# Kernel tuning notes

Hardware: AMD Instinct MI355X
Metric: run time of the kernel (lower is better)

The kernel has to match this reference:

```python
import jax, jax.numpy as jnp
import numpy as np

D_MODEL, N_HEADS, HEAD_DIM, MAX_POS = 1536, 16, 96, 4096
B, T = 2, 2048
BASE = 10000.0


def build_rope3d_Rs(head_dim, max_pos, base=BASE):
    """Rodrigues rotations R(t) = exp(t*M_k): (max_pos, n_trip, 3, 3)."""
    n_trip = head_dim // 3
    inv_freq = base ** (-np.arange(n_trip, dtype=np.float64) * 2.0 / head_dim)
    Ms = np.zeros((n_trip, 3, 3), dtype=np.float64)
    for k in range(n_trip):  # tiny fixed loop (n_trip=32)
        m, axis = inv_freq[k], k % 3
        if axis == 0:
            Ms[k, 0, 1], Ms[k, 1, 0] = m, -m
        elif axis == 1:
            Ms[k, 1, 2], Ms[k, 2, 1] = m, -m
        else:
            Ms[k, 0, 2], Ms[k, 2, 0] = m, -m
    m_s = np.abs(Ms).max(axis=(1, 2))                      # (n_trip,)
    pos = np.arange(max_pos, dtype=np.float64)
    ang = pos[:, None] * m_s[None, :]                      # (P, n_trip)
    Mu = Ms / np.maximum(m_s, 1e-30)[:, None, None]
    Mu2 = np.einsum('kij,kjl->kil', Mu, Mu)
    Rs = (np.eye(3)[None, None]
          + np.sin(ang)[..., None, None] * Mu[None]
          + (1.0 - np.cos(ang))[..., None, None] * Mu2[None])
    return jnp.asarray(Rs, dtype=jnp.float32)


def setup_inputs() -> dict:
    key = jax.random.key(0)
    kx, kq, ko = jax.random.split(key, 3)
    s_in = 1.0 / np.sqrt(D_MODEL)
    s_out = 1.0 / np.sqrt(N_HEADS * HEAD_DIM)
    return {
        'x': jax.random.normal(kx, (B, T, D_MODEL), dtype=jnp.float32),
        'w_qkv': jax.random.normal(kq, (3 * N_HEADS * HEAD_DIM, D_MODEL), dtype=jnp.float32) * s_in,
        'w_o': jax.random.normal(ko, (D_MODEL, N_HEADS * HEAD_DIM), dtype=jnp.float32) * s_out,
        'Rs': build_rope3d_Rs(HEAD_DIM, MAX_POS),
    }


def apply_rope3d(x, Rs):
    # x: (B,H,T,d); Rs: (P, n_trip, 3, 3), d = 3*n_trip
    b, h, t, d = x.shape
    xg = x.reshape(b, h, t, d // 3, 3)
    out = jnp.einsum('tkij,bhtkj->bhtki', Rs[:t], xg)
    return out.reshape(b, h, t, d)


def reference(x, w_qkv, w_o, Rs):
    b, t, _ = x.shape
    qkv = (x @ w_qkv.T).reshape(b, t, 3, N_HEADS, HEAD_DIM)
    qkv = jnp.transpose(qkv, (2, 0, 3, 1, 4))              # (3,B,H,T,hd)
    q, k, v = qkv[0], qkv[1], qkv[2]
    q = apply_rope3d(q, Rs)
    k = apply_rope3d(k, Rs)
    scale = 1.0 / jnp.sqrt(jnp.asarray(HEAD_DIM, dtype=x.dtype))
    scores = jnp.einsum('bhqd,bhkd->bhqk', q, k) * scale   # (B,H,T,T)
    causal = jnp.tril(jnp.ones((t, t), dtype=bool))
    scores = jnp.where(causal, scores, jnp.finfo(x.dtype).min)
    att = jax.nn.softmax(scores, axis=-1)
    out = jnp.einsum('bhqk,bhkd->bhqd', att, v)            # (B,H,T,hd)
    out = jnp.transpose(out, (0, 2, 1, 3)).reshape(b, t, N_HEADS * HEAD_DIM)
    return out @ w_o.T
```

## Files before the change

### kernel.cpp

```cpp
#include <hip/hip_runtime.h>
#include <stdint.h>


typedef unsigned short u16;
typedef unsigned int u32;
typedef __attribute__((ext_vector_type(8))) __bf16 bf16x8;
typedef __attribute__((ext_vector_type(4))) float f32x4;

#define DEV static __device__ __forceinline__

DEV u16 f2bf(float f) {
  u32 u = __float_as_uint(f);
  return (u16)((u + 0x7fffu + ((u >> 16) & 1u)) >> 16);
}
DEV float bf2f(u16 h) { return __uint_as_float(((u32)h) << 16); }
DEV u32 cvtpk(float lo, float hi) {
  u32 r;
  asm("v_cvt_pk_bf16_f32 %0, %1, %2" : "=v"(r) : "v"(lo), "v"(hi));
  return r;
}
DEV float exp2f_fast(float x) {
  float r;
  asm("v_exp_f32 %0, %1" : "=v"(r) : "v"(x));
  return r;
}

DEV void gload16(u16* lds_dst, const u16* gsrc) {
  __builtin_amdgcn_global_load_lds(
      (const __attribute__((address_space(1))) void*)gsrc,
      (__attribute__((address_space(3))) void*)lds_dst, 16, 0, 0);
}

__global__ __launch_bounds__(256) void cvt_bf16(const float* __restrict__ in,
                                                u16* __restrict__ out, int n4) {
  int i = blockIdx.x * 256 + threadIdx.x;
  if (i < n4) {
    float4 v = reinterpret_cast<const float4*>(in)[i];
    ushort4 o;
    o.x = f2bf(v.x); o.y = f2bf(v.y); o.z = f2bf(v.z); o.w = f2bf(v.w);
    reinterpret_cast<ushort4*>(out)[i] = o;
  }
}

template <int OUT_BF16>
__global__ __launch_bounds__(512, 4) void gemm_bal(const u16* __restrict__ A,
                                                   const u16* __restrict__ B,
                                                   void* __restrict__ Cv,
                                                   int M, int N, int K) {
  (void)M;
  __shared__ __align__(16) u16 sA[2][128 * 64];
  __shared__ __align__(16) u16 sB[2][192 * 64];
  const int tid = threadIdx.x;
  const int lane = tid & 63, w = tid >> 6;
  const int wm = w >> 2, wn = w & 3;
  const int fr = lane & 15, fq = lane >> 4;
  const int r0 = blockIdx.x * 128, c0 = blockIdx.y * 192;

  const u16* aSrc[2];
  const u16* bSrc[3];
#pragma unroll
  for (int c = 0; c < 2; ++c) {
    const int idx = c * 512 + tid;
    const int row = idx >> 3;
    aSrc[c] = A + (size_t)(r0 + row) * K + ((idx & 7) ^ (row & 7)) * 8;
  }
#pragma unroll
  for (int c = 0; c < 3; ++c) {
    const int idx = c * 512 + tid;
    const int row = idx >> 3;
    bSrc[c] = B + (size_t)(c0 + row) * K + ((idx & 7) ^ (row & 7)) * 8;
  }

  const int sw0 = ((fq) ^ (fr & 7)) * 8;
  const int sw1 = ((4 + fq) ^ (fr & 7)) * 8;
  const int aB = (wm * 64 + fr) * 64;
  const int bB = (wn * 48 + fr) * 64;

  const f32x4 z4 = {0.f, 0.f, 0.f, 0.f};
  f32x4 acc[4][3];
#pragma unroll
  for (int m = 0; m < 4; ++m)
#pragma unroll
    for (int n = 0; n < 3; ++n) acc[m][n] = z4;

  const int NT = K >> 6;

#define SGA(c, buf, ko) gload16(&sA[buf][((c)*512 + w * 64) * 8], aSrc[c] + (ko))
#define SGB(c, buf, ko) gload16(&sB[buf][((c)*512 + w * 64) * 8], bSrc[c] + (ko))

  SGA(0, 0, 0); SGA(1, 0, 0);
  SGB(0, 0, 0); SGB(1, 0, 0); SGB(2, 0, 0);

  for (int u = 0; u < NT; ++u) {
    const int par = u & 1, nxt = par ^ 1;
    const u16* a = sA[par];
    const u16* b = sB[par];
    const bool pf = (u + 1 < NT);
    const size_t ko = (size_t)(u + 1) * 64;

    asm volatile("s_waitcnt vmcnt(3)" ::: "memory");
    __builtin_amdgcn_s_barrier();
    if (pf) { SGA(0, nxt, ko); SGA(1, nxt, ko); }

    if (pf) { asm volatile("s_waitcnt vmcnt(2)" ::: "memory"); }
    else    { asm volatile("s_waitcnt vmcnt(0)" ::: "memory"); }
    __builtin_amdgcn_s_barrier();
    bf16x8 bfr[3][2];
#pragma unroll
    for (int n = 0; n < 3; ++n) {
      bfr[n][0] = *(const bf16x8*)(b + bB + n * 1024 + sw0);
      bfr[n][1] = *(const bf16x8*)(b + bB + n * 1024 + sw1);
    }
    if (pf) { SGB(0, nxt, ko); SGB(1, nxt, ko); SGB(2, nxt, ko); }
    __builtin_amdgcn_s_barrier();
    __builtin_amdgcn_s_setprio(1);
#pragma unroll
    for (int mp = 0; mp < 2; ++mp) {
      bf16x8 afr[2][2];
#pragma unroll
      for (int i = 0; i < 2; ++i) {
        afr[i][0] = *(const bf16x8*)(a + aB + (2 * mp + i) * 1024 + sw0);
        afr[i][1] = *(const bf16x8*)(a + aB + (2 * mp + i) * 1024 + sw1);
      }
#pragma unroll
      for (int i = 0; i < 2; ++i)
#pragma unroll
        for (int n = 0; n < 3; ++n)
#pragma unroll
          for (int ks = 0; ks < 2; ++ks)
            acc[2 * mp + i][n] = __builtin_amdgcn_mfma_f32_16x16x32_bf16(
                afr[i][ks], bfr[n][ks], acc[2 * mp + i][n], 0, 0, 0);
    }
    __builtin_amdgcn_s_setprio(0);
  }
#undef SGA
#undef SGB

#pragma unroll
  for (int m = 0; m < 4; ++m) {
    const int gr = r0 + wm * 64 + m * 16 + fq * 4;
#pragma unroll
    for (int n = 0; n < 3; ++n) {
      const int gc = c0 + wn * 48 + n * 16 + fr;
#pragma unroll
      for (int j = 0; j < 4; ++j) {
        const size_t off = (size_t)(gr + j) * N + gc;
        if (OUT_BF16) ((u16*)Cv)[off] = f2bf(acc[m][n][j]);
        else          ((float*)Cv)[off] = acc[m][n][j];
      }
    }
  }
}

__global__ __launch_bounds__(256) void rope_kernel(u16* __restrict__ qkv,
                                                   const float* __restrict__ Rs) {
  const int bid = blockIdx.x;
  const int qk = bid & 1;
  const int bt = bid >> 1;
  const int t = bt & 2047;
  const int tid = threadIdx.x;

  __shared__ __align__(16) u16 buf[1536];
  __shared__ __align__(16) float rbuf[288];

  u16* g = qkv + (size_t)bt * 4608 + qk * 1536;
  if (tid < 192)
    *reinterpret_cast<uint4*>(buf + tid * 8) = *reinterpret_cast<const uint4*>(g + tid * 8);
  if (tid < 72)
    *reinterpret_cast<float4*>(rbuf + tid * 4) =
        *reinterpret_cast<const float4*>(Rs + (size_t)t * 288 + tid * 4);
  __syncthreads();

#pragma unroll
  for (int rep = 0; rep < 2; ++rep) {
    const int ft = rep * 256 + tid;
    const int base = (ft >> 5) * 96 + (ft & 31) * 3;
    const float* R = rbuf + (ft & 31) * 9;
    const float x0 = bf2f(buf[base]), x1 = bf2f(buf[base + 1]), x2 = bf2f(buf[base + 2]);
    const float y0 = R[0] * x0 + R[1] * x1 + R[2] * x2;
    const float y1 = R[3] * x0 + R[4] * x1 + R[5] * x2;
    const float y2 = R[6] * x0 + R[7] * x1 + R[8] * x2;
    buf[base] = f2bf(y0); buf[base + 1] = f2bf(y1); buf[base + 2] = f2bf(y2);
  }
  __syncthreads();
  if (tid < 192)
    *reinterpret_cast<uint4*>(g + tid * 8) = *reinterpret_cast<const uint4*>(buf + tid * 8);
}

__global__ __launch_bounds__(256) void kvprep(const u16* __restrict__ qkv,
                                              u16* __restrict__ Kf,
                                              u16* __restrict__ Vf) {
  const int kt = blockIdx.x, bh = blockIdx.y;
  const int b = bh >> 4, h = bh & 15;
  const int tid = threadIdx.x, lane = tid & 63, w = tid >> 6;
  const float SC = 0.14724574f;
  __shared__ __align__(16) u16 vlds[64 * 96];

#pragma unroll
  for (int r = 0; r < 3; ++r) {
    const int idx = r * 256 + tid;
    const int kv = idx / 12, c8 = (idx % 12) * 8;
    gload16(vlds + (r * 256 + w * 64) * 8,
            qkv + (size_t)(b * 2048 + kt * 64 + kv) * 4608 + 3072 + h * 96 + c8);
  }

  const size_t obase = ((size_t)bh * 32 + kt) * 6144;
#pragma unroll
  for (int r = 0; r < 3; ++r) {
    const int chunk = r * 256 + tid;
    const int sub = chunk >> 6, l = chunk & 63;
    const int m = sub / 3, kb = sub % 3;
    const int fr = l & 15, fq = l >> 4;
    uint4 v = *reinterpret_cast<const uint4*>(
        qkv + (size_t)(b * 2048 + kt * 64 + m * 16 + fr) * 4608 + 1536 + h * 96 + kb * 32 + fq * 8);
    u16* p = reinterpret_cast<u16*>(&v);
#pragma unroll
    for (int e = 0; e < 8; ++e) p[e] = f2bf(bf2f(p[e]) * SC);
    *reinterpret_cast<uint4*>(Kf + obase + (size_t)chunk * 8) = v;
  }
  __syncthreads();
#pragma unroll
  for (int r = 0; r < 3; ++r) {
    const int chunk = r * 256 + tid;
    const int sub = chunk >> 6, l = chunk & 63;
    const int n2 = sub >> 1, c = sub & 1;
    const int fr = l & 15, fq = l >> 4;
    const int d = n2 * 16 + fr;
    u16 out[8];
#pragma unroll
    for (int e = 0; e < 8; ++e) {
      const int kl = (c * 2 + (e >> 2)) * 16 + fq * 4 + (e & 3);
      out[e] = vlds[kl * 96 + d];
    }
    *reinterpret_cast<uint4*>(Vf + obase + (size_t)chunk * 8) =
        *reinterpret_cast<uint4*>(out);
  }
}

__global__ __launch_bounds__(256, 2) void attn_fwd(const u16* __restrict__ qkvb,
                                                   const u16* __restrict__ Kf,
                                                   const u16* __restrict__ Vf,
                                                   u16* __restrict__ y) {
  const int bh = blockIdx.x;
  const int qt = 15 - (int)blockIdx.y;
  const int b = bh >> 4, h = bh & 15;
  const int tid = threadIdx.x, lane = tid & 63, w = tid >> 6;
  const int fr = lane & 15, fq = lane >> 4;
  const int q0 = qt * 128;
  const int qw = q0 + w * 32;

  __shared__ __align__(16) u16 kbl[2][6144];
  __shared__ __align__(16) u16 vbl[2][6144];

  bf16x8 qf[2][3];
#pragma unroll
  for (int nq = 0; nq < 2; ++nq)
#pragma unroll
    for (int kb = 0; kb < 3; ++kb)
      qf[nq][kb] = *reinterpret_cast<const bf16x8*>(
          qkvb + (size_t)(b * 2048 + qw + nq * 16 + fr) * 4608 + h * 96 + kb * 32 + fq * 8);

  const f32x4 z4 = {0.f, 0.f, 0.f, 0.f};
  f32x4 oacc[2][6];
#pragma unroll
  for (int mq = 0; mq < 2; ++mq)
#pragma unroll
    for (int n2 = 0; n2 < 6; ++n2) oacc[mq][n2] = z4;
  float mrow[2] = {-1e30f, -1e30f}, ssum[2] = {0.f, 0.f};

  const int nt = 2 * qt + 2;
  const size_t tb = (size_t)bh * 32 * 6144;

#define STAGE(buf, kt_)                                                         \
  do {                                                                          \
    const size_t sb = tb + (size_t)(kt_)*6144;                                  \
    _Pragma("unroll") for (int r = 0; r < 3; ++r) {                             \
      gload16(kbl[buf] + (r * 256 + w * 64) * 8, Kf + sb + (r * 256 + w * 64 + lane) * 8); \
      gload16(vbl[buf] + (r * 256 + w * 64) * 8, Vf + sb + (r * 256 + w * 64 + lane) * 8); \
    }                                                                           \
  } while (0)

  STAGE(0, 0);
  for (int kt = 0; kt < nt; ++kt) {
    __syncthreads();
    if (kt + 1 < nt) STAGE((kt + 1) & 1, kt + 1);
    const u16* kc = kbl[kt & 1];
    const u16* vc = vbl[kt & 1];
    const int k0 = kt * 64;

    if (k0 <= qw + 31) {
      f32x4 sacc[4][2];
#pragma unroll
      for (int m = 0; m < 4; ++m)
#pragma unroll
        for (int nq = 0; nq < 2; ++nq) sacc[m][nq] = z4;
#pragma unroll
      for (int kb = 0; kb < 3; ++kb)
#pragma unroll
        for (int m = 0; m < 4; ++m) {
          const bf16x8 kfrag = *reinterpret_cast<const bf16x8*>(kc + ((m * 3 + kb) * 64 + lane) * 8);
#pragma unroll
          for (int nq = 0; nq < 2; ++nq)
            sacc[m][nq] = __builtin_amdgcn_mfma_f32_16x16x32_bf16(kfrag, qf[nq][kb], sacc[m][nq], 0, 0, 0);
        }
      if (k0 + 63 > qw) {
#pragma unroll
        for (int m = 0; m < 4; ++m) {
          const int kpos = k0 + m * 16 + fq * 4;
#pragma unroll
          for (int nq = 0; nq < 2; ++nq) {
            const int qpos = qw + nq * 16 + fr;
#pragma unroll
            for (int j = 0; j < 4; ++j)
              if (kpos + j > qpos) sacc[m][nq][j] = -1e30f;
          }
        }
      }
      float al[2];
#pragma unroll
      for (int nq = 0; nq < 2; ++nq) {
        float mx = sacc[0][nq][0];
#pragma unroll
        for (int m = 0; m < 4; ++m)
#pragma unroll
          for (int j = 0; j < 4; ++j) mx = fmaxf(mx, sacc[m][nq][j]);
        mx = fmaxf(mx, __shfl_xor(mx, 16));
        mx = fmaxf(mx, __shfl_xor(mx, 32));
        const float mn = fmaxf(mrow[nq], mx);
        al[nq] = exp2f_fast(mrow[nq] - mn);
        mrow[nq] = mn;
        float s = 0.f;
#pragma unroll
        for (int m = 0; m < 4; ++m) {
          f32x4 p;
#pragma unroll
          for (int j = 0; j < 4; ++j) p[j] = exp2f_fast(sacc[m][nq][j] - mn);
          sacc[m][nq] = p;
          s += (p[0] + p[1]) + (p[2] + p[3]);
        }
        s += __shfl_xor(s, 16);
        s += __shfl_xor(s, 32);
        ssum[nq] = ssum[nq] * al[nq] + s;
      }
      float alb[2][4];
#pragma unroll
      for (int mq = 0; mq < 2; ++mq)
#pragma unroll
        for (int j = 0; j < 4; ++j) alb[mq][j] = __shfl(al[mq], fq * 4 + j);
#pragma unroll
      for (int mq = 0; mq < 2; ++mq)
#pragma unroll
        for (int n2 = 0; n2 < 6; ++n2) {
          f32x4 t = oacc[mq][n2];
          t[0] *= alb[mq][0]; t[1] *= alb[mq][1]; t[2] *= alb[mq][2]; t[3] *= alb[mq][3];
          oacc[mq][n2] = t;
        }
      union PB { u32 u[4]; bf16x8 v; };
      PB pa[2][2];
#pragma unroll
      for (int c = 0; c < 2; ++c)
#pragma unroll
        for (int mq = 0; mq < 2; ++mq) {
          pa[c][mq].u[0] = cvtpk(sacc[2 * c][mq][0], sacc[2 * c][mq][1]);
          pa[c][mq].u[1] = cvtpk(sacc[2 * c][mq][2], sacc[2 * c][mq][3]);
          pa[c][mq].u[2] = cvtpk(sacc[2 * c + 1][mq][0], sacc[2 * c + 1][mq][1]);
          pa[c][mq].u[3] = cvtpk(sacc[2 * c + 1][mq][2], sacc[2 * c + 1][mq][3]);
        }
#pragma unroll
      for (int c = 0; c < 2; ++c)
#pragma unroll
        for (int n2 = 0; n2 < 6; ++n2) {
          const bf16x8 vfrag = *reinterpret_cast<const bf16x8*>(vc + ((n2 * 2 + c) * 64 + lane) * 8);
#pragma unroll
          for (int mq = 0; mq < 2; ++mq)
            oacc[mq][n2] = __builtin_amdgcn_mfma_f32_16x16x32_bf16(pa[c][mq].v, vfrag, oacc[mq][n2], 0, 0, 0);
        }
    }
  }
#undef STAGE

  float inv[2][4];
#pragma unroll
  for (int mq = 0; mq < 2; ++mq)
#pragma unroll
    for (int j = 0; j < 4; ++j)
      inv[mq][j] = __builtin_amdgcn_rcpf(__shfl(ssum[mq], fq * 4 + j));
#pragma unroll
  for (int mq = 0; mq < 2; ++mq)
#pragma unroll
    for (int n2 = 0; n2 < 6; ++n2)
#pragma unroll
      for (int j = 0; j < 4; ++j) {
        const size_t off =
            (size_t)(b * 2048 + qw + mq * 16 + fq * 4 + j) * 1536 + h * 96 + n2 * 16 + fr;
        y[off] = f2bf(oacc[mq][n2][j] * inv[mq][j]);
      }
}

extern "C" void kernel_launch(void* const* d_in, const int* in_sizes, int n_in,
                              void* d_out, int out_size, void* d_ws, size_t ws_size,
                              hipStream_t stream) {
  (void)in_sizes; (void)n_in; (void)out_size; (void)ws_size;
  const float* x     = (const float*)d_in[0];
  const float* w_qkv = (const float*)d_in[1];
  const float* w_o   = (const float*)d_in[2];
  const float* Rs    = (const float*)d_in[3];
  float* out = (float*)d_out;

  u16* xb    = (u16*)d_ws;
  u16* wqkvb = xb + 6291456;
  u16* wob   = xb + 13369344;
  u16* qkvb  = xb + 15728640;
  u16* yb    = xb + 34603008;
  u16* Kf    = xb;
  u16* Vf    = xb + 6291456;

  cvt_bf16<<<1572864 / 256, 256, 0, stream>>>(x, xb, 1572864);
  cvt_bf16<<<1769472 / 256, 256, 0, stream>>>(w_qkv, wqkvb, 1769472);
  cvt_bf16<<<589824 / 256, 256, 0, stream>>>(w_o, wob, 589824);

  gemm_bal<1><<<dim3(32, 24), 512, 0, stream>>>(xb, wqkvb, (void*)qkvb, 4096, 4608, 1536);
  rope_kernel<<<8192, 256, 0, stream>>>(qkvb, Rs);
  kvprep<<<dim3(32, 32), 256, 0, stream>>>(qkvb, Kf, Vf);
  attn_fwd<<<dim3(32, 16), 256, 0, stream>>>(qkvb, Kf, Vf, yb);
  gemm_bal<0><<<dim3(32, 8), 512, 0, stream>>>(yb, wob, (void*)out, 4096, 1536, 1536);
}
```

Baseline: 295.3 us.

## Merge conversion launches, widen rope blocks, lazy softmax rescale with MFMA row sums

The three fp32-to-bf16 conversion launches become one kernel. The rope kernel now handles both q and k of a token per block, halving the block count. In attention, max uses 3-input max ops, and the running max and output rescale are updated only when some row's new max exceeds the old by more than 8 (log2 domain). The row sums are computed by an extra MFMA against a ones vector, replacing shuffle reductions. This cuts per-tile VALU and shuffle work but adds MFMA work and accumulator registers, and it allows exponentials up to 2^8 before rescaling.

Result: faster. 272.7 us (-7.6%).

```diff
diff --git a/kernel.cpp b/kernel.cpp
--- a/kernel.cpp
+++ b/kernel.cpp
@@ -24,6 +24,7 @@
   asm("v_exp_f32 %0, %1" : "=v"(r) : "v"(x));
   return r;
 }
+DEV float max3f(float a, float b, float c) { return fmaxf(fmaxf(a, b), c); }
 
 DEV void gload16(u16* lds_dst, const u16* gsrc) {
   __builtin_amdgcn_global_load_lds(
@@ -31,15 +32,20 @@
       (__attribute__((address_space(3))) void*)lds_dst, 16, 0, 0);
 }
 
-__global__ __launch_bounds__(256) void cvt_bf16(const float* __restrict__ in,
-                                                u16* __restrict__ out, int n4) {
+__global__ __launch_bounds__(256) void cvt3(const float* __restrict__ a, u16* __restrict__ ao, int na4,
+                                            const float* __restrict__ b, u16* __restrict__ bo, int nb4,
+                                            const float* __restrict__ c, u16* __restrict__ co, int nc4) {
   int i = blockIdx.x * 256 + threadIdx.x;
-  if (i < n4) {
-    float4 v = reinterpret_cast<const float4*>(in)[i];
-    ushort4 o;
-    o.x = f2bf(v.x); o.y = f2bf(v.y); o.z = f2bf(v.z); o.w = f2bf(v.w);
-    reinterpret_cast<ushort4*>(out)[i] = o;
-  }
+  const float* src;
+  u16* dst;
+  if (i < na4) { src = a; dst = ao; }
+  else if (i < na4 + nb4) { i -= na4; src = b; dst = bo; }
+  else if (i < na4 + nb4 + nc4) { i -= na4 + nb4; src = c; dst = co; }
+  else return;
+  float4 v = reinterpret_cast<const float4*>(src)[i];
+  ushort4 o;
+  o.x = f2bf(v.x); o.y = f2bf(v.y); o.z = f2bf(v.z); o.w = f2bf(v.w);
+  reinterpret_cast<ushort4*>(dst)[i] = o;
 }
 
 template <int OUT_BF16>
@@ -154,27 +160,29 @@
 
 __global__ __launch_bounds__(256) void rope_kernel(u16* __restrict__ qkv,
                                                    const float* __restrict__ Rs) {
-  const int bid = blockIdx.x;
-  const int qk = bid & 1;
-  const int bt = bid >> 1;
+  const int bt = blockIdx.x;
   const int t = bt & 2047;
   const int tid = threadIdx.x;
 
-  __shared__ __align__(16) u16 buf[1536];
+  __shared__ __align__(16) u16 buf[3072];
   __shared__ __align__(16) float rbuf[288];
 
-  u16* g = qkv + (size_t)bt * 4608 + qk * 1536;
-  if (tid < 192)
-    *reinterpret_cast<uint4*>(buf + tid * 8) = *reinterpret_cast<const uint4*>(g + tid * 8);
+  u16* g = qkv + (size_t)bt * 4608;
+#pragma unroll
+  for (int r = 0; r < 2; ++r) {
+    const int idx = r * 256 + tid;
+    if (idx < 384)
+      *reinterpret_cast<uint4*>(buf + idx * 8) = *reinterpret_cast<const uint4*>(g + idx * 8);
+  }
   if (tid < 72)
     *reinterpret_cast<float4*>(rbuf + tid * 4) =
         *reinterpret_cast<const float4*>(Rs + (size_t)t * 288 + tid * 4);
   __syncthreads();
 
 #pragma unroll
-  for (int rep = 0; rep < 2; ++rep) {
+  for (int rep = 0; rep < 4; ++rep) {
     const int ft = rep * 256 + tid;
-    const int base = (ft >> 5) * 96 + (ft & 31) * 3;
+    const int base = (ft >> 9) * 1536 + ((ft & 511) >> 5) * 96 + (ft & 31) * 3;
     const float* R = rbuf + (ft & 31) * 9;
     const float x0 = bf2f(buf[base]), x1 = bf2f(buf[base + 1]), x2 = bf2f(buf[base + 2]);
     const float y0 = R[0] * x0 + R[1] * x1 + R[2] * x2;
@@ -183,8 +191,12 @@
     buf[base] = f2bf(y0); buf[base + 1] = f2bf(y1); buf[base + 2] = f2bf(y2);
   }
   __syncthreads();
-  if (tid < 192)
-    *reinterpret_cast<uint4*>(g + tid * 8) = *reinterpret_cast<const uint4*>(buf + tid * 8);
+#pragma unroll
+  for (int r = 0; r < 2; ++r) {
+    const int idx = r * 256 + tid;
+    if (idx < 384)
+      *reinterpret_cast<uint4*>(g + idx * 8) = *reinterpret_cast<const uint4*>(buf + idx * 8);
+  }
 }
 
 __global__ __launch_bounds__(256) void kvprep(const u16* __restrict__ qkv,
@@ -260,13 +272,19 @@
       qf[nq][kb] = *reinterpret_cast<const bf16x8*>(
           qkvb + (size_t)(b * 2048 + qw + nq * 16 + fr) * 4608 + h * 96 + kb * 32 + fq * 8);
 
+  union OneU { u16 s[8]; bf16x8 v; };
+  OneU ou;
+#pragma unroll
+  for (int e = 0; e < 8; ++e) ou.s[e] = 0x3f80;
+  const bf16x8 vones = ou.v;
+
   const f32x4 z4 = {0.f, 0.f, 0.f, 0.f};
-  f32x4 oacc[2][6];
+  f32x4 oacc[2][7];
 #pragma unroll
   for (int mq = 0; mq < 2; ++mq)
 #pragma unroll
-    for (int n2 = 0; n2 < 6; ++n2) oacc[mq][n2] = z4;
-  float mrow[2] = {-1e30f, -1e30f}, ssum[2] = {0.f, 0.f};
+    for (int n2 = 0; n2 < 7; ++n2) oacc[mq][n2] = z4;
+  float mrow[2] = {-1e30f, -1e30f};
 
   const int nt = 2 * qt + 2;
   const size_t tb = (size_t)bh * 32 * 6144;
@@ -316,44 +334,50 @@
           }
         }
       }
-      float al[2];
+      float mx[2];
 #pragma unroll
       for (int nq = 0; nq < 2; ++nq) {
-        float mx = sacc[0][nq][0];
-#pragma unroll
-        for (int m = 0; m < 4; ++m)
-#pragma unroll
-          for (int j = 0; j < 4; ++j) mx = fmaxf(mx, sacc[m][nq][j]);
-        mx = fmaxf(mx, __shfl_xor(mx, 16));
-        mx = fmaxf(mx, __shfl_xor(mx, 32));
-        const float mn = fmaxf(mrow[nq], mx);
-        al[nq] = exp2f_fast(mrow[nq] - mn);
-        mrow[nq] = mn;
-        float s = 0.f;
+        const float t0 = max3f(sacc[0][nq][0], sacc[0][nq][1], sacc[0][nq][2]);
+        const float t1 = max3f(sacc[0][nq][3], sacc[1][nq][0], sacc[1][nq][1]);
+        const float t2 = max3f(sacc[1][nq][2], sacc[1][nq][3], sacc[2][nq][0]);
+        const float t3 = max3f(sacc[2][nq][1], sacc[2][nq][2], sacc[2][nq][3]);
+        const float t4 = max3f(sacc[3][nq][0], sacc[3][nq][1], sacc[3][nq][2]);
+        float m = max3f(max3f(t0, t1, t2), t3, max3f(t4, sacc[3][nq][3], t0));
+        m = fmaxf(m, __shfl_xor(m, 16));
+        m = fmaxf(m, __shfl_xor(m, 32));
+        mx[nq] = m;
+      }
+      const bool need = (mx[0] - mrow[0] > 8.0f) || (mx[1] - mrow[1] > 8.0f);
+      if (__any(need)) {
+        float al[2];
+#pragma unroll
+        for (int nq = 0; nq < 2; ++nq) {
+          const float mn = fmaxf(mrow[nq], mx[nq]);
+          al[nq] = exp2f_fast(mrow[nq] - mn);
+          mrow[nq] = mn;
+        }
+        float alb[2][4];
+#pragma unroll
+        for (int mq = 0; mq < 2; ++mq)
+#pragma unroll
+          for (int j = 0; j < 4; ++j) alb[mq][j] = __shfl(al[mq], fq * 4 + j);
+#pragma unroll
+        for (int mq = 0; mq < 2; ++mq)
+#pragma unroll
+          for (int n2 = 0; n2 < 7; ++n2) {
+            f32x4 t = oacc[mq][n2];
+            t[0] *= alb[mq][0]; t[1] *= alb[mq][1]; t[2] *= alb[mq][2]; t[3] *= alb[mq][3];
+            oacc[mq][n2] = t;
+          }
+      }
+#pragma unroll
+      for (int nq = 0; nq < 2; ++nq)
 #pragma unroll
         for (int m = 0; m < 4; ++m) {
           f32x4 p;
 #pragma unroll
-          for (int j = 0; j < 4; ++j) p[j] = exp2f_fast(sacc[m][nq][j] - mn);
+          for (int j = 0; j < 4; ++j) p[j] = exp2f_fast(sacc[m][nq][j] - mrow[nq]);
           sacc[m][nq] = p;
-          s += (p[0] + p[1]) + (p[2] + p[3]);
-        }
-        s += __shfl_xor(s, 16);
-        s += __shfl_xor(s, 32);
-        ssum[nq] = ssum[nq] * al[nq] + s;
-      }
-      float alb[2][4];
-#pragma unroll
-      for (int mq = 0; mq < 2; ++mq)
-#pragma unroll
-        for (int j = 0; j < 4; ++j) alb[mq][j] = __shfl(al[mq], fq * 4 + j);
-#pragma unroll
-      for (int mq = 0; mq < 2; ++mq)
-#pragma unroll
-        for (int n2 = 0; n2 < 6; ++n2) {
-          f32x4 t = oacc[mq][n2];
-          t[0] *= alb[mq][0]; t[1] *= alb[mq][1]; t[2] *= alb[mq][2]; t[3] *= alb[mq][3];
-          oacc[mq][n2] = t;
         }
       union PB { u32 u[4]; bf16x8 v; };
       PB pa[2][2];
@@ -369,8 +393,10 @@
 #pragma unroll
       for (int c = 0; c < 2; ++c)
 #pragma unroll
-        for (int n2 = 0; n2 < 6; ++n2) {
-          const bf16x8 vfrag = *reinterpret_cast<const bf16x8*>(vc + ((n2 * 2 + c) * 64 + lane) * 8);
+        for (int n2 = 0; n2 < 7; ++n2) {
+          const bf16x8 vfrag = (n2 < 6)
+              ? *reinterpret_cast<const bf16x8*>(vc + ((n2 * 2 + c) * 64 + lane) * 8)
+              : vones;
 #pragma unroll
           for (int mq = 0; mq < 2; ++mq)
             oacc[mq][n2] = __builtin_amdgcn_mfma_f32_16x16x32_bf16(pa[c][mq].v, vfrag, oacc[mq][n2], 0, 0, 0);
@@ -384,7 +410,7 @@
   for (int mq = 0; mq < 2; ++mq)
 #pragma unroll
     for (int j = 0; j < 4; ++j)
-      inv[mq][j] = __builtin_amdgcn_rcpf(__shfl(ssum[mq], fq * 4 + j));
+      inv[mq][j] = __builtin_amdgcn_rcpf(oacc[mq][6][j]);
 #pragma unroll
   for (int mq = 0; mq < 2; ++mq)
 #pragma unroll
@@ -415,12 +441,11 @@
   u16* Kf    = xb;
   u16* Vf    = xb + 6291456;
 
-  cvt_bf16<<<1572864 / 256, 256, 0, stream>>>(x, xb, 1572864);
-  cvt_bf16<<<1769472 / 256, 256, 0, stream>>>(w_qkv, wqkvb, 1769472);
-  cvt_bf16<<<589824 / 256, 256, 0, stream>>>(w_o, wob, 589824);
+  cvt3<<<(1572864 + 1769472 + 589824) / 256, 256, 0, stream>>>(
+      x, xb, 1572864, w_qkv, wqkvb, 1769472, w_o, wob, 589824);
 
   gemm_bal<1><<<dim3(32, 24), 512, 0, stream>>>(xb, wqkvb, (void*)qkvb, 4096, 4608, 1536);
-  rope_kernel<<<8192, 256, 0, stream>>>(qkvb, Rs);
+  rope_kernel<<<4096, 256, 0, stream>>>(qkvb, Rs);
   kvprep<<<dim3(32, 32), 256, 0, stream>>>(qkvb, Kf, Vf);
   attn_fwd<<<dim3(32, 16), 256, 0, stream>>>(qkvb, Kf, Vf, yb);
   gemm_bal<0><<<dim3(32, 8), 512, 0, stream>>>(yb, wob, (void*)out, 4096, 1536, 1536);
```
